# Performance work log

Hardware: AMD Instinct MI355X
Metric: run time of the kernel (lower is better)

## Reference

```python
import jax, jax.numpy as jnp
import numpy as np

LOG2 = float(np.log(2.0))
N_NODES = 100000

def ssp(x):
    return jax.nn.softplus(x) - LOG2

def _xavier(key, out_dim, in_dim):
    bound = float(np.sqrt(6.0 / (in_dim + out_dim)))
    return jax.random.uniform(key, (out_dim, in_dim), jnp.float32, -bound, bound)

def setup_inputs() -> dict:
    key = jax.random.key(0)
    ks = jax.random.split(key, 10)
    H, F = 128, 128  # hidden_channels, num_filters
    C2 = int(2 * H * 0.5)          # lin2 out = 128
    C2h = int(2 * H) - C2          # lin2_hull out = 128
    E, Eh = 1600000, 400000
    v = jax.random.normal(ks[0], (N_NODES, H), jnp.float32)
    e = jax.random.normal(ks[1], (E, F), jnp.float32)
    edge_index = jax.random.randint(ks[2], (2, E), 0, N_NODES, jnp.int64)
    e_hull = jax.random.normal(ks[3], (Eh, F), jnp.float32)
    edge_index_hull = jax.random.randint(ks[4], (2, Eh), 0, N_NODES, jnp.int64)
    return {
        "v": v, "e": e, "edge_index": edge_index,
        "e_hull": e_hull, "edge_index_hull": edge_index_hull,
        "W1": _xavier(ks[5], H, F), "b1": jnp.zeros((H,), jnp.float32),
        "W2": _xavier(ks[6], C2, H), "b2": jnp.zeros((C2,), jnp.float32),
        "W1h": _xavier(ks[7], H, F), "b1h": jnp.zeros((H,), jnp.float32),
        "W2h": _xavier(ks[8], C2h, H), "b2h": jnp.zeros((C2h,), jnp.float32),
        "Wc": _xavier(ks[9], H, C2 + C2h), "bc": jnp.zeros((H,), jnp.float32),
    }

def reference(v, e, edge_index, e_hull, edge_index_hull,
              W1, b1, W2, b2, W1h, b1h, W2h, b2h, Wc, bc):
    n = v.shape[0]
    i = edge_index[1]
    out = jax.ops.segment_sum(e, i, num_segments=n)          # [N, F] scatter-sum
    out = ssp(out @ W1.T + b1) @ W2.T + b2                   # [N, C2]
    i_ = edge_index_hull[1]
    out_hull = jax.ops.segment_sum(e_hull, i_, num_segments=n)
    out_hull = ssp(out_hull @ W1h.T + b1h) @ W2h.T + b2h     # [N, C2h]
    cat = jnp.concatenate([out, out_hull], axis=1)           # [N, C2+C2h]
    return v + ssp(cat @ Wc.T + bc)
```

## Files before the change

### kernel.cpp

```cpp
#include <hip/hip_runtime.h>
#include <math.h>

typedef __attribute__((ext_vector_type(8))) short short8;
typedef __attribute__((ext_vector_type(4))) float f32x4;
typedef unsigned short u16;
typedef unsigned int u32;

__device__ __forceinline__ float ssp(float x) {
    float ax = fabsf(x);
    return fmaxf(x, 0.0f) + __logf(1.0f + __expf(-ax)) - 0.69314718055994530942f;
}

__device__ __forceinline__ u16 f2bf(float x) {
    u32 u = __float_as_uint(x);
    u32 r = (u + 0x7FFFu + ((u >> 16) & 1u)) >> 16;
    return (u16)r;
}

__global__ __launch_bounds__(256) void hist_kernel(
    const int* __restrict__ tgt, int* __restrict__ counts, int E)
{
    int i = blockIdx.x * 256 + threadIdx.x;
    if (i < E) atomicAdd(&counts[tgt[i]], 1);
}

__global__ __launch_bounds__(1024) void scan1_kernel(
    const int* __restrict__ counts, int* __restrict__ offsets,
    int* __restrict__ bsums, int n)
{
    __shared__ int buf[2][1024];
    const int tid = threadIdx.x;
    const int idx = blockIdx.x * 1024 + tid;
    int val = (idx < n) ? counts[idx] : 0;
    int cur = 0;
    buf[0][tid] = val;
    __syncthreads();
    for (int off = 1; off < 1024; off <<= 1) {
        int x = buf[cur][tid];
        if (tid >= off) x += buf[cur][tid - off];
        buf[cur ^ 1][tid] = x;
        cur ^= 1;
        __syncthreads();
    }
    if (idx < n) offsets[idx] = buf[cur][tid] - val;
    if (tid == 1023) bsums[blockIdx.x] = buf[cur][tid];
}

__global__ __launch_bounds__(128) void scan2_kernel(
    int* __restrict__ bsums, int nb, int* __restrict__ offsets, int n)
{
    __shared__ int b[2][128];
    const int tid = threadIdx.x;
    int val = (tid < nb) ? bsums[tid] : 0;
    int cur = 0;
    b[0][tid] = val;
    __syncthreads();
    for (int off = 1; off < 128; off <<= 1) {
        int x = b[cur][tid];
        if (tid >= off) x += b[cur][tid - off];
        b[cur ^ 1][tid] = x;
        cur ^= 1;
        __syncthreads();
    }
    if (tid < nb) bsums[tid] = b[cur][tid] - val;
    if (tid == 127) offsets[n] = b[cur][127];
}

__global__ __launch_bounds__(256) void scan3_kernel(
    int* __restrict__ offsets, const int* __restrict__ bsums, int n)
{
    int idx = blockIdx.x * 256 + threadIdx.x;
    if (idx < n) offsets[idx] += bsums[idx >> 10];
}

__global__ __launch_bounds__(256) void place_kernel(
    const int* __restrict__ tgt, const int* __restrict__ offsets,
    int* __restrict__ cursors, int* __restrict__ perm, int E)
{
    int i = blockIdx.x * 256 + threadIdx.x;
    if (i < E) {
        int node = tgt[i];
        int pos = offsets[node] + atomicAdd(&cursors[node], 1);
        perm[pos] = i;
    }
}

__global__ __launch_bounds__(256) void gather_kernel(
    const float* __restrict__ e, const int* __restrict__ perm,
    const int* __restrict__ offsets, u16* __restrict__ acc, int n)
{
    int node = blockIdx.x * 8 + (threadIdx.x >> 5);
    if (node >= n) return;
    int c4 = threadIdx.x & 31;
    int s0 = offsets[node], s1 = offsets[node + 1];
    float4 s = make_float4(0.f, 0.f, 0.f, 0.f);
    int k = s0;
    for (; k + 2 <= s1; k += 2) {
        int e0 = perm[k], e1 = perm[k + 1];
        float4 a = ((const float4*)e)[(long long)e0 * 32 + c4];
        float4 b = ((const float4*)e)[(long long)e1 * 32 + c4];
        s.x += a.x; s.y += a.y; s.z += a.z; s.w += a.w;
        s.x += b.x; s.y += b.y; s.z += b.z; s.w += b.w;
    }
    if (k < s1) {
        float4 a = ((const float4*)e)[(long long)perm[k] * 32 + c4];
        s.x += a.x; s.y += a.y; s.z += a.z; s.w += a.w;
    }
    ushort4 o;
    o.x = f2bf(s.x); o.y = f2bf(s.y); o.z = f2bf(s.z); o.w = f2bf(s.w);
    *(ushort4*)&acc[(long long)node * 128 + c4 * 4] = o;
}

__global__ __launch_bounds__(256) void wconvert_kernel(
    const float* __restrict__ W1, const float* __restrict__ W1h,
    const float* __restrict__ W2, const float* __restrict__ W2h,
    const float* __restrict__ Wc, u16* __restrict__ dst)
{
    int i = blockIdx.x * 256 + threadIdx.x;
    if (i >= 98304) return;
    const float* src; int off;
    if      (i < 16384) { src = W1;  off = i; }
    else if (i < 32768) { src = W1h; off = i - 16384; }
    else if (i < 49152) { src = W2;  off = i - 32768; }
    else if (i < 65536) { src = W2h; off = i - 49152; }
    else                { src = Wc;  off = i - 65536; }
    dst[i] = f2bf(src[off]);
}

#define MT 64

#define CHUNK_IDX(row, ch) (((row) * 16 + ((ch) ^ ((row) & 7))))
#define AFRAG(ls, row, ch) (*(const short8*)&(ls)[CHUNK_IDX(row, ch) * 8])

__device__ __forceinline__ void layer128(
    const u16* __restrict__ ls, const u16* __restrict__ W,
    const float* __restrict__ bias, u16* __restrict__ dst,
    int rw, int lr, int kc, bool act)
{
    const int arow = rw + lr;
    short8 af[4];
    #pragma unroll
    for (int s = 0; s < 4; s++) af[s] = AFRAG(ls, arow, s * 4 + kc);
    #pragma unroll
    for (int nt = 0; nt < 8; nt++) {
        const int bcol = nt * 16 + lr;
        const short8* wr = (const short8*)(W + bcol * 128);
        f32x4 acc = {0.f, 0.f, 0.f, 0.f};
        #pragma unroll
        for (int s = 0; s < 4; s++)
            acc = __builtin_amdgcn_mfma_f32_16x16x32_bf16(af[s], wr[s * 4 + kc], acc, 0, 0, 0);
        const float bn = bias[bcol];
        #pragma unroll
        for (int r = 0; r < 4; r++) {
            const int drow = rw + kc * 4 + r;
            float val = acc[r] + bn;
            if (act) val = ssp(val);
            dst[CHUNK_IDX(drow, bcol >> 3) * 8 + (bcol & 7)] = f2bf(val);
        }
    }
}

__global__ __launch_bounds__(256) void mlp_mfma_kernel(
    const u16* __restrict__ accm, const u16* __restrict__ acch,
    const u16* __restrict__ Wbf,
    const float* __restrict__ b1, const float* __restrict__ b1h,
    const float* __restrict__ b2, const float* __restrict__ b2h,
    const float* __restrict__ bc,
    const float* __restrict__ v, float* __restrict__ out, int n)
{
    __shared__ __align__(16) u16 lsA[MT * 128];
    __shared__ __align__(16) u16 lsB[MT * 128];
    __shared__ __align__(16) u16 lsC[MT * 128];
    __shared__ __align__(16) u16 lsD[MT * 128];

    const int tid = threadIdx.x;
    const int l   = tid & 63;
    const int w   = tid >> 6;
    const int rw  = w * 16;
    const int lr  = l & 15;
    const int kc  = l >> 4;
    const int node0 = blockIdx.x * MT;

    const u16* W1  = Wbf;
    const u16* W1h = Wbf + 16384;
    const u16* W2  = Wbf + 32768;
    const u16* W2h = Wbf + 49152;
    const u16* Wc  = Wbf + 65536;

    for (int p = tid; p < 1024; p += 256) {
        int row = p >> 4, c = p & 15;
        int4 a = make_int4(0, 0, 0, 0), b = a;
        if (node0 + row < n) {
            a = ((const int4*)accm)[(size_t)(node0 + row) * 16 + c];
            b = ((const int4*)acch)[(size_t)(node0 + row) * 16 + c];
        }
        ((int4*)lsA)[CHUNK_IDX(row, c)] = a;
        ((int4*)lsB)[CHUNK_IDX(row, c)] = b;
    }
    __syncthreads();

    layer128(lsA, W1,  b1,  lsC, rw, lr, kc, true);
    layer128(lsB, W1h, b1h, lsD, rw, lr, kc, true);
    __syncthreads();

    layer128(lsC, W2,  b2,  lsA, rw, lr, kc, false);
    layer128(lsD, W2h, b2h, lsB, rw, lr, kc, false);
    __syncthreads();

    {
        const int arow = rw + lr;
        short8 af[8];
        #pragma unroll
        for (int s = 0; s < 4; s++) af[s]     = AFRAG(lsA, arow, s * 4 + kc);
        #pragma unroll
        for (int s = 0; s < 4; s++) af[s + 4] = AFRAG(lsB, arow, s * 4 + kc);
        #pragma unroll
        for (int nt = 0; nt < 8; nt++) {
            const int bcol = nt * 16 + lr;
            const short8* wr = (const short8*)(Wc + bcol * 256);
            f32x4 acc = {0.f, 0.f, 0.f, 0.f};
            #pragma unroll
            for (int s = 0; s < 8; s++)
                acc = __builtin_amdgcn_mfma_f32_16x16x32_bf16(af[s], wr[s * 4 + kc], acc, 0, 0, 0);
            const float bn = bc[bcol];
            #pragma unroll
            for (int r = 0; r < 4; r++) {
                const int drow = rw + kc * 4 + r;
                const int node = node0 + drow;
                if (node < n) {
                    size_t off = (size_t)node * 128 + bcol;
                    out[off] = v[off] + ssp(acc[r] + bn);
                }
            }
        }
    }
}

extern "C" void kernel_launch(void* const* d_in, const int* in_sizes, int n_in,
                              void* d_out, int out_size, void* d_ws, size_t ws_size,
                              hipStream_t stream)
{
    const float* v    = (const float*)d_in[0];
    const float* e    = (const float*)d_in[1];
    const int*   ei   = (const int*)  d_in[2];
    const float* eh   = (const float*)d_in[3];
    const int*   eih  = (const int*)  d_in[4];
    const float* W1   = (const float*)d_in[5];
    const float* b1   = (const float*)d_in[6];
    const float* W2   = (const float*)d_in[7];
    const float* b2   = (const float*)d_in[8];
    const float* W1h  = (const float*)d_in[9];
    const float* b1h  = (const float*)d_in[10];
    const float* W2h  = (const float*)d_in[11];
    const float* b2h  = (const float*)d_in[12];
    const float* Wc   = (const float*)d_in[13];
    const float* bc   = (const float*)d_in[14];
    float* out = (float*)d_out;

    const int N  = in_sizes[0] / 128;
    const int E  = (int)(in_sizes[1] / 128);
    const int Eh = (int)(in_sizes[3] / 128);

    u16* accm = (u16*)d_ws;
    u16* acch = accm + (size_t)N * 128;
    u16* Wbf  = acch + (size_t)N * 128;
    int* counts  = (int*)(Wbf + 98304);
    int* cursors = counts + N;
    int* offsets = cursors + N;
    int* bsums   = offsets + (N + 1);
    int* perm    = bsums + 128;

    const int* tgt_m = ei  + E;
    const int* tgt_h = eih + Eh;

    const int NB = (N + 1023) / 1024;

    wconvert_kernel<<<(98304 + 255) / 256, 256, 0, stream>>>(W1, W1h, W2, W2h, Wc, Wbf);

    hipMemsetAsync(counts, 0, (size_t)2 * N * 4, stream);
    hist_kernel <<<(E + 255) / 256, 256, 0, stream>>>(tgt_m, counts, E);
    scan1_kernel<<<NB, 1024, 0, stream>>>(counts, offsets, bsums, N);
    scan2_kernel<<<1, 128, 0, stream>>>(bsums, NB, offsets, N);
    scan3_kernel<<<(N + 255) / 256, 256, 0, stream>>>(offsets, bsums, N);
    place_kernel<<<(E + 255) / 256, 256, 0, stream>>>(tgt_m, offsets, cursors, perm, E);
    gather_kernel<<<(N + 7) / 8, 256, 0, stream>>>(e, perm, offsets, accm, N);

    hipMemsetAsync(counts, 0, (size_t)2 * N * 4, stream);
    hist_kernel <<<(Eh + 255) / 256, 256, 0, stream>>>(tgt_h, counts, Eh);
    scan1_kernel<<<NB, 1024, 0, stream>>>(counts, offsets, bsums, N);
    scan2_kernel<<<1, 128, 0, stream>>>(bsums, NB, offsets, N);
    scan3_kernel<<<(N + 255) / 256, 256, 0, stream>>>(offsets, bsums, N);
    place_kernel<<<(Eh + 255) / 256, 256, 0, stream>>>(tgt_h, offsets, cursors, perm, Eh);
    gather_kernel<<<(N + 7) / 8, 256, 0, stream>>>(eh, perm, offsets, acch, N);

    mlp_mfma_kernel<<<(N + MT - 1) / MT, 256, 0, stream>>>(
        accm, acch, Wbf, b1, b1h, b2, b2h, bc, v, out, N);
}
```

Measured before the change: 653.3 us.

## Merge main and hull CSR build and gather into single combined passes

```diff
diff --git a/kernel.cpp b/kernel.cpp
--- a/kernel.cpp
+++ b/kernel.cpp
@@ -17,11 +17,14 @@
     return (u16)r;
 }
 
-__global__ __launch_bounds__(256) void hist_kernel(
-    const int* __restrict__ tgt, int* __restrict__ counts, int E)
+__global__ __launch_bounds__(256) void hist2_kernel(
+    const int* __restrict__ tgt_m, int E,
+    const int* __restrict__ tgt_h, int Eh,
+    int* __restrict__ counts, int N)
 {
     int i = blockIdx.x * 256 + threadIdx.x;
-    if (i < E) atomicAdd(&counts[tgt[i]], 1);
+    if (i < E) atomicAdd(&counts[tgt_m[i]], 1);
+    else if (i < E + Eh) atomicAdd(&counts[N + tgt_h[i - E]], 1);
 }
 
 __global__ __launch_bounds__(1024) void scan1_kernel(
@@ -46,16 +49,16 @@
     if (tid == 1023) bsums[blockIdx.x] = buf[cur][tid];
 }
 
-__global__ __launch_bounds__(128) void scan2_kernel(
+__global__ __launch_bounds__(256) void scan2_kernel(
     int* __restrict__ bsums, int nb, int* __restrict__ offsets, int n)
 {
-    __shared__ int b[2][128];
+    __shared__ int b[2][256];
     const int tid = threadIdx.x;
     int val = (tid < nb) ? bsums[tid] : 0;
     int cur = 0;
     b[0][tid] = val;
     __syncthreads();
-    for (int off = 1; off < 128; off <<= 1) {
+    for (int off = 1; off < 256; off <<= 1) {
         int x = b[cur][tid];
         if (tid >= off) x += b[cur][tid - off];
         b[cur ^ 1][tid] = x;
@@ -63,7 +66,7 @@
         __syncthreads();
     }
     if (tid < nb) bsums[tid] = b[cur][tid] - val;
-    if (tid == 127) offsets[n] = b[cur][127];
+    if (tid == 255) offsets[n] = b[cur][255];
 }
 
 __global__ __launch_bounds__(256) void scan3_kernel(
@@ -73,42 +76,61 @@
     if (idx < n) offsets[idx] += bsums[idx >> 10];
 }
 
-__global__ __launch_bounds__(256) void place_kernel(
-    const int* __restrict__ tgt, const int* __restrict__ offsets,
-    int* __restrict__ cursors, int* __restrict__ perm, int E)
+__global__ __launch_bounds__(256) void place2_kernel(
+    const int* __restrict__ tgt_m, int E,
+    const int* __restrict__ tgt_h, int Eh,
+    const int* __restrict__ offsets, int* __restrict__ cursors,
+    int* __restrict__ perm, int N)
 {
     int i = blockIdx.x * 256 + threadIdx.x;
     if (i < E) {
-        int node = tgt[i];
-        int pos = offsets[node] + atomicAdd(&cursors[node], 1);
+        int slot = tgt_m[i];
+        int pos = offsets[slot] + atomicAdd(&cursors[slot], 1);
         perm[pos] = i;
+    } else if (i < E + Eh) {
+        int slot = N + tgt_h[i - E];
+        int pos = offsets[slot] + atomicAdd(&cursors[slot], 1);
+        perm[pos] = i - E;
     }
 }
 
 __global__ __launch_bounds__(256) void gather_kernel(
-    const float* __restrict__ e, const int* __restrict__ perm,
-    const int* __restrict__ offsets, u16* __restrict__ acc, int n)
-{
-    int node = blockIdx.x * 8 + (threadIdx.x >> 5);
-    if (node >= n) return;
-    int c4 = threadIdx.x & 31;
-    int s0 = offsets[node], s1 = offsets[node + 1];
-    float4 s = make_float4(0.f, 0.f, 0.f, 0.f);
+    const float* __restrict__ e, const float* __restrict__ eh,
+    const int* __restrict__ perm, const int* __restrict__ offsets,
+    u16* __restrict__ accm, u16* __restrict__ acch, int n)
+{
+    int slot = blockIdx.x * 8 + (threadIdx.x >> 5);
+    if (slot >= 2 * n) return;
+    const int c4 = threadIdx.x & 31;
+    const bool hull = slot >= n;
+    const f32x4* src = (const f32x4*)(hull ? eh : e);
+    const int node = hull ? slot - n : slot;
+    u16* dst = hull ? acch : accm;
+
+    int s0 = offsets[slot], s1 = offsets[slot + 1];
+    f32x4 s = {0.f, 0.f, 0.f, 0.f};
     int k = s0;
+    for (; k + 4 <= s1; k += 4) {
+        int p0 = perm[k], p1 = perm[k + 1], p2 = perm[k + 2], p3 = perm[k + 3];
+        f32x4 a = __builtin_nontemporal_load(&src[(size_t)p0 * 32 + c4]);
+        f32x4 b = __builtin_nontemporal_load(&src[(size_t)p1 * 32 + c4]);
+        f32x4 c = __builtin_nontemporal_load(&src[(size_t)p2 * 32 + c4]);
+        f32x4 d = __builtin_nontemporal_load(&src[(size_t)p3 * 32 + c4]);
+        s += a + b + c + d;
+    }
     for (; k + 2 <= s1; k += 2) {
-        int e0 = perm[k], e1 = perm[k + 1];
-        float4 a = ((const float4*)e)[(long long)e0 * 32 + c4];
-        float4 b = ((const float4*)e)[(long long)e1 * 32 + c4];
-        s.x += a.x; s.y += a.y; s.z += a.z; s.w += a.w;
-        s.x += b.x; s.y += b.y; s.z += b.z; s.w += b.w;
+        int p0 = perm[k], p1 = perm[k + 1];
+        f32x4 a = __builtin_nontemporal_load(&src[(size_t)p0 * 32 + c4]);
+        f32x4 b = __builtin_nontemporal_load(&src[(size_t)p1 * 32 + c4]);
+        s += a + b;
     }
     if (k < s1) {
-        float4 a = ((const float4*)e)[(long long)perm[k] * 32 + c4];
-        s.x += a.x; s.y += a.y; s.z += a.z; s.w += a.w;
+        f32x4 a = __builtin_nontemporal_load(&src[(size_t)perm[k] * 32 + c4]);
+        s += a;
     }
     ushort4 o;
     o.x = f2bf(s.x); o.y = f2bf(s.y); o.z = f2bf(s.z); o.w = f2bf(s.w);
-    *(ushort4*)&acc[(long long)node * 128 + c4 * 4] = o;
+    *(ushort4*)&dst[(size_t)node * 128 + c4 * 4] = o;
 }
 
 __global__ __launch_bounds__(256) void wconvert_kernel(
@@ -260,38 +282,32 @@
     const int N  = in_sizes[0] / 128;
     const int E  = (int)(in_sizes[1] / 128);
     const int Eh = (int)(in_sizes[3] / 128);
+    const int n2 = 2 * N;
 
     u16* accm = (u16*)d_ws;
     u16* acch = accm + (size_t)N * 128;
     u16* Wbf  = acch + (size_t)N * 128;
     int* counts  = (int*)(Wbf + 98304);
-    int* cursors = counts + N;
-    int* offsets = cursors + N;
-    int* bsums   = offsets + (N + 1);
-    int* perm    = bsums + 128;
+    int* cursors = counts + n2;
+    int* offsets = cursors + n2;
+    int* bsums   = offsets + (n2 + 1);
+    int* perm    = bsums + 256;
 
     const int* tgt_m = ei  + E;
     const int* tgt_h = eih + Eh;
 
-    const int NB = (N + 1023) / 1024;
+    const int NB  = (n2 + 1023) / 1024;
+    const int ET  = E + Eh;
 
     wconvert_kernel<<<(98304 + 255) / 256, 256, 0, stream>>>(W1, W1h, W2, W2h, Wc, Wbf);
 
-    hipMemsetAsync(counts, 0, (size_t)2 * N * 4, stream);
-    hist_kernel <<<(E + 255) / 256, 256, 0, stream>>>(tgt_m, counts, E);
-    scan1_kernel<<<NB, 1024, 0, stream>>>(counts, offsets, bsums, N);
-    scan2_kernel<<<1, 128, 0, stream>>>(bsums, NB, offsets, N);
-    scan3_kernel<<<(N + 255) / 256, 256, 0, stream>>>(offsets, bsums, N);
-    place_kernel<<<(E + 255) / 256, 256, 0, stream>>>(tgt_m, offsets, cursors, perm, E);
-    gather_kernel<<<(N + 7) / 8, 256, 0, stream>>>(e, perm, offsets, accm, N);
-
-    hipMemsetAsync(counts, 0, (size_t)2 * N * 4, stream);
-    hist_kernel <<<(Eh + 255) / 256, 256, 0, stream>>>(tgt_h, counts, Eh);
-    scan1_kernel<<<NB, 1024, 0, stream>>>(counts, offsets, bsums, N);
-    scan2_kernel<<<1, 128, 0, stream>>>(bsums, NB, offsets, N);
-    scan3_kernel<<<(N + 255) / 256, 256, 0, stream>>>(offsets, bsums, N);
-    place_kernel<<<(Eh + 255) / 256, 256, 0, stream>>>(tgt_h, offsets, cursors, perm, Eh);
-    gather_kernel<<<(N + 7) / 8, 256, 0, stream>>>(eh, perm, offsets, acch, N);
+    (void)hipMemsetAsync(counts, 0, (size_t)2 * n2 * 4, stream);
+    hist2_kernel <<<(ET + 255) / 256, 256, 0, stream>>>(tgt_m, E, tgt_h, Eh, counts, N);
+    scan1_kernel <<<NB, 1024, 0, stream>>>(counts, offsets, bsums, n2);
+    scan2_kernel <<<1, 256, 0, stream>>>(bsums, NB, offsets, n2);
+    scan3_kernel <<<(n2 + 255) / 256, 256, 0, stream>>>(offsets, bsums, n2);
+    place2_kernel<<<(ET + 255) / 256, 256, 0, stream>>>(tgt_m, E, tgt_h, Eh, offsets, cursors, perm, N);
+    gather_kernel<<<(n2 + 7) / 8, 256, 0, stream>>>(e, eh, perm, offsets, accm, acch, N);
 
     mlp_mfma_kernel<<<(N + MT - 1) / MT, 256, 0, stream>>>(
         accm, acch, Wbf, b1, b1h, b2, b2h, bc, v, out, N);
```

Result: faster. 613.7 us (-6.1%).
